# Performance work log

Hardware: AMD Instinct MI355X
Metric: run time of the kernel (lower is better)

The kernel has to match this reference:

```python
import jax, jax.numpy as jnp
import numpy as np

N = 50000      # nodes
E = 800000     # edges
IN = 128       # in_ch
OUT = 32       # out_ch
H = 4          # heads
ED = 16        # edge_dim
SLOPE = 0.2    # LeakyReLU negative slope (GATv2 default and outer activation)


def setup_inputs() -> dict:
    key = jax.random.key(0)
    ks = jax.random.split(key, 10)
    s_in = 1.0 / np.sqrt(IN)
    s_ed = 1.0 / np.sqrt(ED)
    s_out = 1.0 / np.sqrt(OUT)
    return {
        "x": jax.random.normal(ks[0], (N, IN), jnp.float32),
        "edge_index": jax.random.randint(ks[1], (2, E), 0, N, dtype=jnp.int32),
        "edges_attr": jax.random.normal(ks[2], (E, ED), jnp.float32),
        "W_l": jax.random.normal(ks[3], (IN, H * OUT), jnp.float32) * s_in,
        "b_l": jnp.zeros((H * OUT,), jnp.float32),
        "W_r": jax.random.normal(ks[4], (IN, H * OUT), jnp.float32) * s_in,
        "b_r": jnp.zeros((H * OUT,), jnp.float32),
        "W_e": jax.random.normal(ks[5], (ED, H * OUT), jnp.float32) * s_ed,
        "att": jax.random.normal(ks[6], (H, OUT), jnp.float32) * s_out,
        "bias": jnp.zeros((OUT,), jnp.float32),
    }


def reference(x, edge_index, edges_attr, W_l, b_l, W_r, b_r, W_e, att, bias):
    src, tgt = edge_index[0], edge_index[1]

    # add_self_loops with fill_value='mean': self-loop attr = scatter-mean of
    # incoming edge attrs per target node (0 for isolated nodes, as in PyG).
    deg = jax.ops.segment_sum(jnp.ones((E,), x.dtype), tgt, num_segments=N)
    attr_sum = jax.ops.segment_sum(edges_attr, tgt, num_segments=N)
    loop_attr = attr_sum / jnp.maximum(deg, 1.0)[:, None]
    node_ids = jnp.arange(N, dtype=src.dtype)
    src_f = jnp.concatenate([src, node_ids])   # [E+N]
    tgt_f = jnp.concatenate([tgt, node_ids])   # [E+N]
    attr_f = jnp.concatenate([edges_attr, loop_attr], axis=0)  # [E+N, ED]

    x_l = (x @ W_l + b_l).reshape(N, H, OUT)   # source transform
    x_r = (x @ W_r + b_r).reshape(N, H, OUT)   # target transform
    e = (attr_f @ W_e).reshape(-1, H, OUT)     # edge transform

    # GATv2 score: att . leaky_relu(x_l[j] + x_r[i] + e_ij)
    m = x_l[src_f] + x_r[tgt_f] + e                          # [E+N, H, OUT]
    scores = jnp.einsum('ehc,hc->eh', jax.nn.leaky_relu(m, SLOPE), att)

    # scatter-softmax over edges grouped by target node (every segment has a
    # self-loop, so segment_max is well-defined)
    smax = jax.ops.segment_max(scores, tgt_f, num_segments=N)
    ex = jnp.exp(scores - smax[tgt_f])
    denom = jax.ops.segment_sum(ex, tgt_f, num_segments=N)
    alpha = ex / denom[tgt_f]                                # [E+N, H]

    # weighted aggregation of source messages x_l[j]
    msg = alpha[:, :, None] * x_l[src_f]                     # [E+N, H, OUT]
    out = jax.ops.segment_sum(msg, tgt_f, num_segments=N)   # [N, H, OUT]

    out = out.mean(axis=1) + bias                            # concat=False -> head mean
    return jax.nn.leaky_relu(out, SLOPE)                     # outer LeakyReLU(0.2)
```

## Files before the change

### kernel.cpp

```cpp
#include <hip/hip_runtime.h>
#include <math.h>

#define NN 50000
#define NE 800000
#define SLOPE 0.2f
#define NB 49


__global__ void deg_kernel(const int* __restrict__ tgt, int* __restrict__ deg) {
  int e = blockIdx.x * 256 + threadIdx.x;
  if (e < NE) atomicAdd(&deg[tgt[e]], 1);
}

__global__ void partial_kernel(const int* __restrict__ deg, int* __restrict__ psum) {
  int b = blockIdx.x;
  int base = b * 1024 + threadIdx.x * 4;
  int s = 0;
  if (base + 3 < NN) {
    int4 v = *(const int4*)(deg + base);
    s = v.x + v.y + v.z + v.w;
  } else {
#pragma unroll
    for (int i = 0; i < 4; ++i)
      if (base + i < NN) s += deg[base + i];
  }
  s += __shfl_xor(s, 1);
  s += __shfl_xor(s, 2);
  s += __shfl_xor(s, 4);
  s += __shfl_xor(s, 8);
  s += __shfl_xor(s, 16);
  s += __shfl_xor(s, 32);
  __shared__ int wsum[4];
  if ((threadIdx.x & 63) == 0) wsum[threadIdx.x >> 6] = s;
  __syncthreads();
  if (threadIdx.x == 0) psum[b] = wsum[0] + wsum[1] + wsum[2] + wsum[3];
}

__global__ void scanpart_kernel(const int* __restrict__ psum, int* __restrict__ offs,
                                int* __restrict__ rowptr) {
  int lane = threadIdx.x;
  int mine = (lane < NB) ? psum[lane] : 0;
  int v = mine;
#pragma unroll
  for (int off = 1; off < 64; off <<= 1) {
    int u = __shfl_up(v, off);
    if (lane >= off) v += u;
  }
  if (lane < NB) offs[lane] = v - mine;
  if (lane == 63) rowptr[NN] = v;
}

__global__ void final_kernel(const int* __restrict__ deg, const int* __restrict__ offs,
                             int* __restrict__ rowptr, int* __restrict__ cursor) {
  int b = blockIdx.x;
  int t = threadIdx.x;
  int base = b * 1024 + t * 4;
  int d0 = 0, d1 = 0, d2 = 0, d3 = 0;
  if (base + 3 < NN) {
    int4 v = *(const int4*)(deg + base);
    d0 = v.x; d1 = v.y; d2 = v.z; d3 = v.w;
  } else {
    if (base < NN) d0 = deg[base];
    if (base + 1 < NN) d1 = deg[base + 1];
    if (base + 2 < NN) d2 = deg[base + 2];
  }
  int s = d0 + d1 + d2 + d3;
  int lane = t & 63, w = t >> 6;
  int v = s;
#pragma unroll
  for (int off = 1; off < 64; off <<= 1) {
    int u = __shfl_up(v, off);
    if (lane >= off) v += u;
  }
  __shared__ int wtot[4];
  if (lane == 63) wtot[w] = v;
  __syncthreads();
  int woff = 0;
#pragma unroll
  for (int i = 0; i < 4; ++i)
    if (i < w) woff += wtot[i];
  int run = offs[b] + woff + (v - s);
  if (base < NN)     { rowptr[base] = run;     cursor[base] = run;     run += d0; }
  if (base + 1 < NN) { rowptr[base + 1] = run; cursor[base + 1] = run; run += d1; }
  if (base + 2 < NN) { rowptr[base + 2] = run; cursor[base + 2] = run; run += d2; }
  if (base + 3 < NN) { rowptr[base + 3] = run; cursor[base + 3] = run; }
}

__global__ void scatter_kernel(const int* __restrict__ src, const int* __restrict__ tgt,
                               int* __restrict__ cursor, int2* __restrict__ csr) {
  int e = blockIdx.x * 256 + threadIdx.x;
  if (e < NE) {
    int t = tgt[e];
    int pos = atomicAdd(&cursor[t], 1);
    csr[pos] = make_int2(src[e], e);
  }
}


__launch_bounds__(256)
__global__ void gemm_kernel(const float* __restrict__ x,
                            const float* __restrict__ W_l, const float* __restrict__ b_l,
                            const float* __restrict__ W_r, const float* __restrict__ b_r,
                            float* __restrict__ x_l, float* __restrict__ x_r) {
  __shared__ float xs[64 * 68];
  __shared__ float wsm[64 * 128];
  int tid = threadIdx.x;
  int cx = tid & 31;
  int rn = tid >> 5;
  int n0 = blockIdx.x * 64;
  bool isL = (blockIdx.y == 0);
  const float* W = isL ? W_l : W_r;

  float acc[8][4];
#pragma unroll
  for (int i = 0; i < 8; ++i)
#pragma unroll
    for (int j = 0; j < 4; ++j) acc[i][j] = 0.f;

  for (int kb = 0; kb < 128; kb += 64) {
#pragma unroll
    for (int r = 0; r < 4; ++r) {
      int q = tid + r * 256;
      int n = q >> 4, k4 = q & 15;
      float4 v = make_float4(0.f, 0.f, 0.f, 0.f);
      int gn = n0 + n;
      if (gn < NN) v = *(const float4*)(x + (size_t)gn * 128 + kb + 4 * k4);
      *(float4*)&xs[n * 68 + 4 * k4] = v;
    }
#pragma unroll
    for (int r = 0; r < 8; ++r) {
      int q = tid + r * 256;
      int kk = q >> 5, c4 = q & 31;
      float4 wv = *(const float4*)(W + (size_t)(kb + kk) * 128 + 4 * c4);
      *(float4*)&wsm[kk * 128 + 4 * c4] = wv;
    }
    __syncthreads();
#pragma unroll 2
    for (int k4 = 0; k4 < 16; ++k4) {
      float4 wv[4];
#pragma unroll
      for (int kk = 0; kk < 4; ++kk)
        wv[kk] = *(const float4*)&wsm[(4 * k4 + kk) * 128 + 4 * cx];
#pragma unroll
      for (int i = 0; i < 8; ++i) {
        float4 xv = *(const float4*)&xs[(8 * rn + i) * 68 + 4 * k4];
        acc[i][0] = fmaf(xv.x, wv[0].x, acc[i][0]);
        acc[i][1] = fmaf(xv.x, wv[0].y, acc[i][1]);
        acc[i][2] = fmaf(xv.x, wv[0].z, acc[i][2]);
        acc[i][3] = fmaf(xv.x, wv[0].w, acc[i][3]);
        acc[i][0] = fmaf(xv.y, wv[1].x, acc[i][0]);
        acc[i][1] = fmaf(xv.y, wv[1].y, acc[i][1]);
        acc[i][2] = fmaf(xv.y, wv[1].z, acc[i][2]);
        acc[i][3] = fmaf(xv.y, wv[1].w, acc[i][3]);
        acc[i][0] = fmaf(xv.z, wv[2].x, acc[i][0]);
        acc[i][1] = fmaf(xv.z, wv[2].y, acc[i][1]);
        acc[i][2] = fmaf(xv.z, wv[2].z, acc[i][2]);
        acc[i][3] = fmaf(xv.z, wv[2].w, acc[i][3]);
        acc[i][0] = fmaf(xv.w, wv[3].x, acc[i][0]);
        acc[i][1] = fmaf(xv.w, wv[3].y, acc[i][1]);
        acc[i][2] = fmaf(xv.w, wv[3].z, acc[i][2]);
        acc[i][3] = fmaf(xv.w, wv[3].w, acc[i][3]);
      }
    }
    __syncthreads();
  }

  const float* bptr = isL ? b_l : b_r;
  float* optr = isL ? x_l : x_r;
  int cc = 4 * cx;
  float4 bv = *(const float4*)(bptr + cc);
#pragma unroll
  for (int i = 0; i < 8; ++i) {
    int gn = n0 + 8 * rn + i;
    if (gn < NN) {
      float4 o = make_float4(acc[i][0] + bv.x, acc[i][1] + bv.y,
                             acc[i][2] + bv.z, acc[i][3] + bv.w);
      *(float4*)(optr + (size_t)gn * 128 + cc) = o;
    }
  }
}


#define EDGE_PROC(AV, XL)                                              \
  {                                                                    \
    float e0 = AV[0] * wek[0].x;                                       \
    e0 = fmaf(AV[1], wek[1].x, e0);   e0 = fmaf(AV[2], wek[2].x, e0);  \
    e0 = fmaf(AV[3], wek[3].x, e0);   e0 = fmaf(AV[4], wek[4].x, e0);  \
    e0 = fmaf(AV[5], wek[5].x, e0);   e0 = fmaf(AV[6], wek[6].x, e0);  \
    e0 = fmaf(AV[7], wek[7].x, e0);   e0 = fmaf(AV[8], wek[8].x, e0);  \
    e0 = fmaf(AV[9], wek[9].x, e0);   e0 = fmaf(AV[10], wek[10].x, e0);\
    e0 = fmaf(AV[11], wek[11].x, e0); e0 = fmaf(AV[12], wek[12].x, e0);\
    e0 = fmaf(AV[13], wek[13].x, e0); e0 = fmaf(AV[14], wek[14].x, e0);\
    e0 = fmaf(AV[15], wek[15].x, e0);                                  \
    float e1 = AV[0] * wek[0].y;                                       \
    e1 = fmaf(AV[1], wek[1].y, e1);   e1 = fmaf(AV[2], wek[2].y, e1);  \
    e1 = fmaf(AV[3], wek[3].y, e1);   e1 = fmaf(AV[4], wek[4].y, e1);  \
    e1 = fmaf(AV[5], wek[5].y, e1);   e1 = fmaf(AV[6], wek[6].y, e1);  \
    e1 = fmaf(AV[7], wek[7].y, e1);   e1 = fmaf(AV[8], wek[8].y, e1);  \
    e1 = fmaf(AV[9], wek[9].y, e1);   e1 = fmaf(AV[10], wek[10].y, e1);\
    e1 = fmaf(AV[11], wek[11].y, e1); e1 = fmaf(AV[12], wek[12].y, e1);\
    e1 = fmaf(AV[13], wek[13].y, e1); e1 = fmaf(AV[14], wek[14].y, e1);\
    e1 = fmaf(AV[15], wek[15].y, e1);                                  \
    es0 += e0; es1 += e1;                                              \
    float m0 = (XL.x + xr.x) + e0;                                     \
    float m1 = (XL.y + xr.y) + e1;                                     \
    float lm0 = fmaf(SLOPE, fminf(m0, 0.f), fmaxf(m0, 0.f));           \
    float lm1 = fmaf(SLOPE, fminf(m1, 0.f), fmaxf(m1, 0.f));           \
    float part = fmaf(attv.y, lm1, attv.x * lm0);                      \
    part += __shfl_xor(part, 1);                                       \
    part += __shfl_xor(part, 2);                                       \
    part += __shfl_xor(part, 4);                                       \
    part += __shfl_xor(part, 8);                                       \
    float p = __expf(part);                                            \
    lh += p;                                                           \
    acc0 = fmaf(p, XL.x, acc0);                                        \
    acc1 = fmaf(p, XL.y, acc1);                                        \
  }

__launch_bounds__(256)
__global__ void gat_kernel(const float* __restrict__ x_l, const float* __restrict__ x_r,
                           const int* __restrict__ rowptr, const int2* __restrict__ csr,
                           const float* __restrict__ eattr, const float* __restrict__ W_e,
                           const float* __restrict__ att, const float* __restrict__ bias,
                           float* __restrict__ out) {
  int wid = threadIdx.x >> 6;
  int lane = threadIdx.x & 63;
  int tbase = (blockIdx.x * 4 + wid) * 4;

  float2 wek[16];
#pragma unroll
  for (int k = 0; k < 16; ++k)
    wek[k] = *(const float2*)(W_e + k * 128 + 2 * lane);
  float2 attv = *(const float2*)(att + 2 * lane);
  float bv = bias[(2 * lane) & 31];
  float bv1 = bias[((2 * lane) & 31) + 1];

  for (int tt = 0; tt < 4; ++tt) {
    int t = tbase + tt;
    float2 xr = *(const float2*)(x_r + (size_t)t * 128 + 2 * lane);
    int start = __builtin_amdgcn_readfirstlane(rowptr[t]);
    int end = __builtin_amdgcn_readfirstlane(rowptr[t + 1]);

    float lh = 0.f, acc0 = 0.f, acc1 = 0.f, es0 = 0.f, es1 = 0.f;

    int j = start;
    for (; j + 2 <= end; j += 2) {
      int2 ceA = csr[j];
      int2 ceB = csr[j + 1];
      int srcA = __builtin_amdgcn_readfirstlane(ceA.x);
      int eidA = __builtin_amdgcn_readfirstlane(ceA.y);
      int srcB = __builtin_amdgcn_readfirstlane(ceB.x);
      int eidB = __builtin_amdgcn_readfirstlane(ceB.y);
      const float* apA = eattr + (size_t)eidA * 16;
      const float* apB = eattr + (size_t)eidB * 16;
      float aA[16], aB[16];
#pragma unroll
      for (int k = 0; k < 16; ++k) aA[k] = apA[k];
#pragma unroll
      for (int k = 0; k < 16; ++k) aB[k] = apB[k];
      float2 xlA = *(const float2*)(x_l + (size_t)srcA * 128 + 2 * lane);
      float2 xlB = *(const float2*)(x_l + (size_t)srcB * 128 + 2 * lane);
      EDGE_PROC(aA, xlA)
      EDGE_PROC(aB, xlB)
    }
    if (j < end) {
      int2 ce = csr[j];
      int srcn = __builtin_amdgcn_readfirstlane(ce.x);
      int eid = __builtin_amdgcn_readfirstlane(ce.y);
      const float* ap = eattr + (size_t)eid * 16;
      float aC[16];
#pragma unroll
      for (int k = 0; k < 16; ++k) aC[k] = ap[k];
      float2 xlC = *(const float2*)(x_l + (size_t)srcn * 128 + 2 * lane);
      EDGE_PROC(aC, xlC)
    }

    {
      float rdeg = 1.0f / fmaxf((float)(end - start), 1.0f);
      float e0 = es0 * rdeg, e1 = es1 * rdeg;
      float2 xl = *(const float2*)(x_l + (size_t)t * 128 + 2 * lane);
      float m0 = (xl.x + xr.x) + e0;
      float m1 = (xl.y + xr.y) + e1;
      float lm0 = fmaf(SLOPE, fminf(m0, 0.f), fmaxf(m0, 0.f));
      float lm1 = fmaf(SLOPE, fminf(m1, 0.f), fmaxf(m1, 0.f));
      float part = fmaf(attv.y, lm1, attv.x * lm0);
      part += __shfl_xor(part, 1);
      part += __shfl_xor(part, 2);
      part += __shfl_xor(part, 4);
      part += __shfl_xor(part, 8);
      float p = __expf(part);
      lh += p;
      acc0 = fmaf(p, xl.x, acc0);
      acc1 = fmaf(p, xl.y, acc1);
    }

    float inv = 1.0f / lh;
    float v0 = acc0 * inv, v1 = acc1 * inv;
    v0 += __shfl_xor(v0, 16);
    v0 += __shfl_xor(v0, 32);
    v1 += __shfl_xor(v1, 16);
    v1 += __shfl_xor(v1, 32);
    if (lane < 16) {
      float o0 = fmaf(v0, 0.25f, bv);
      float o1 = fmaf(v1, 0.25f, bv1);
      o0 = fmaf(SLOPE, fminf(o0, 0.f), fmaxf(o0, 0.f));
      o1 = fmaf(SLOPE, fminf(o1, 0.f), fmaxf(o1, 0.f));
      *(float2*)(out + (size_t)t * 32 + 2 * lane) = make_float2(o0, o1);
    }
  }
}


extern "C" void kernel_launch(void* const* d_in, const int* in_sizes, int n_in,
                              void* d_out, int out_size, void* d_ws, size_t ws_size,
                              hipStream_t stream) {
  const float* x = (const float*)d_in[0];
  const int* ei = (const int*)d_in[1];
  const float* eattr = (const float*)d_in[2];
  const float* W_l = (const float*)d_in[3];
  const float* b_l = (const float*)d_in[4];
  const float* W_r = (const float*)d_in[5];
  const float* b_r = (const float*)d_in[6];
  const float* W_e = (const float*)d_in[7];
  const float* att = (const float*)d_in[8];
  const float* bias = (const float*)d_in[9];
  float* out = (float*)d_out;

  char* ws = (char*)d_ws;
  int2* csr = (int2*)ws;
  float* x_l = (float*)(ws + 6400000);
  float* x_r = (float*)(ws + 32000000);
  int* deg = (int*)(ws + 57600000);
  int* rowptr = (int*)(ws + 57800000);
  int* cursor = (int*)(ws + 58000016);
  int* psum = (int*)(ws + 58200016);
  int* offs = (int*)(ws + 58200512);

  hipMemsetAsync(deg, 0, NN * sizeof(int), stream);
  deg_kernel<<<(NE + 255) / 256, 256, 0, stream>>>(ei + NE, deg);
  partial_kernel<<<NB, 256, 0, stream>>>(deg, psum);
  scanpart_kernel<<<1, 64, 0, stream>>>(psum, offs, rowptr);
  final_kernel<<<NB, 256, 0, stream>>>(deg, offs, rowptr, cursor);
  scatter_kernel<<<(NE + 255) / 256, 256, 0, stream>>>(ei, ei + NE, cursor, csr);
  gemm_kernel<<<dim3((NN + 63) / 64, 2), 256, 0, stream>>>(x, W_l, b_l, W_r, b_r, x_l, x_r);
  gat_kernel<<<NN / 16, 256, 0, stream>>>(x_l, x_r, rowptr, csr, eattr, W_e, att, bias, out);
}
```

Before: 348.4 us.

## Permute edge attributes into CSR order during scatter and stream them sequentially

Result: slower. 372.9 us (+7.0%).

```diff
diff --git a/kernel.cpp b/kernel.cpp
--- a/kernel.cpp
+++ b/kernel.cpp
@@ -5,6 +5,7 @@
 #define NE 800000
 #define SLOPE 0.2f
 #define NB 49
+#define LOG2E 1.44269504f
 
 
 __global__ void deg_kernel(const int* __restrict__ tgt, int* __restrict__ deg) {
@@ -86,8 +87,28 @@
   if (base + 3 < NN) { rowptr[base + 3] = run; cursor[base + 3] = run; }
 }
 
-__global__ void scatter_kernel(const int* __restrict__ src, const int* __restrict__ tgt,
-                               int* __restrict__ cursor, int2* __restrict__ csr) {
+__global__ void scatter_attr_kernel(const int* __restrict__ src, const int* __restrict__ tgt,
+                                    const float4* __restrict__ ea4, int* __restrict__ cursor,
+                                    int* __restrict__ csr_src, float4* __restrict__ attr_csr) {
+  int e = blockIdx.x * 256 + threadIdx.x;
+  if (e < NE) {
+    float4 a0 = ea4[(size_t)e * 4 + 0];
+    float4 a1 = ea4[(size_t)e * 4 + 1];
+    float4 a2 = ea4[(size_t)e * 4 + 2];
+    float4 a3 = ea4[(size_t)e * 4 + 3];
+    int t = tgt[e];
+    int pos = atomicAdd(&cursor[t], 1);
+    csr_src[pos] = src[e];
+    size_t b = (size_t)pos * 4;
+    attr_csr[b + 0] = a0;
+    attr_csr[b + 1] = a1;
+    attr_csr[b + 2] = a2;
+    attr_csr[b + 3] = a3;
+  }
+}
+
+__global__ void scatter_eid_kernel(const int* __restrict__ src, const int* __restrict__ tgt,
+                                   int* __restrict__ cursor, int2* __restrict__ csr) {
   int e = blockIdx.x * 256 + threadIdx.x;
   if (e < NE) {
     int t = tgt[e];
@@ -176,6 +197,123 @@
       float4 o = make_float4(acc[i][0] + bv.x, acc[i][1] + bv.y,
                              acc[i][2] + bv.z, acc[i][3] + bv.w);
       *(float4*)(optr + (size_t)gn * 128 + cc) = o;
+    }
+  }
+}
+
+
+__launch_bounds__(256)
+__global__ void gat_seq_kernel(const float* __restrict__ x_l, const float* __restrict__ x_r,
+                               const int* __restrict__ rowptr, const int* __restrict__ csr_src,
+                               const float4* __restrict__ attr4, const float* __restrict__ W_e,
+                               const float* __restrict__ att, const float* __restrict__ bias,
+                               float* __restrict__ out) {
+  int wid = threadIdx.x >> 6;
+  int lane = threadIdx.x & 63;
+  int tbase = (blockIdx.x * 4 + wid) * 4;
+
+  float2 wek[16];
+#pragma unroll
+  for (int k = 0; k < 16; ++k)
+    wek[k] = *(const float2*)(W_e + k * 128 + 2 * lane);
+  float2 attv = *(const float2*)(att + 2 * lane);
+  attv.x *= LOG2E;
+  attv.y *= LOG2E;
+  float bv0 = bias[(2 * lane) & 31];
+  float bv1 = bias[((2 * lane) & 31) + 1];
+
+  for (int tt = 0; tt < 4; ++tt) {
+    int t = tbase + tt;
+    float2 xr = *(const float2*)(x_r + (size_t)t * 128 + 2 * lane);
+    int start = __builtin_amdgcn_readfirstlane(rowptr[t]);
+    int end = __builtin_amdgcn_readfirstlane(rowptr[t + 1]);
+
+    float lh = 0.f, acc0 = 0.f, acc1 = 0.f, es0 = 0.f, es1 = 0.f;
+
+    if (end > start) {
+      int s0 = __builtin_amdgcn_readfirstlane(csr_src[start]);
+      float2 xl = *(const float2*)(x_l + (size_t)s0 * 128 + 2 * lane);
+      int j1 = (start + 1 < end) ? start + 1 : start;
+      int svn = csr_src[j1];
+
+      for (int j = start; j < end; ++j) {
+        size_t ab = (size_t)j * 4;
+        float4 A0 = attr4[ab + 0];
+        float4 A1 = attr4[ab + 1];
+        float4 A2 = attr4[ab + 2];
+        float4 A3 = attr4[ab + 3];
+        int sn = __builtin_amdgcn_readfirstlane(svn);
+        float2 nxl = *(const float2*)(x_l + (size_t)sn * 128 + 2 * lane);
+        int jnn = (j + 2 < end) ? j + 2 : start;
+        svn = csr_src[jnn];
+
+        float e0 = A0.x * wek[0].x;
+        e0 = fmaf(A0.y, wek[1].x, e0);  e0 = fmaf(A0.z, wek[2].x, e0);
+        e0 = fmaf(A0.w, wek[3].x, e0);  e0 = fmaf(A1.x, wek[4].x, e0);
+        e0 = fmaf(A1.y, wek[5].x, e0);  e0 = fmaf(A1.z, wek[6].x, e0);
+        e0 = fmaf(A1.w, wek[7].x, e0);  e0 = fmaf(A2.x, wek[8].x, e0);
+        e0 = fmaf(A2.y, wek[9].x, e0);  e0 = fmaf(A2.z, wek[10].x, e0);
+        e0 = fmaf(A2.w, wek[11].x, e0); e0 = fmaf(A3.x, wek[12].x, e0);
+        e0 = fmaf(A3.y, wek[13].x, e0); e0 = fmaf(A3.z, wek[14].x, e0);
+        e0 = fmaf(A3.w, wek[15].x, e0);
+        float e1 = A0.x * wek[0].y;
+        e1 = fmaf(A0.y, wek[1].y, e1);  e1 = fmaf(A0.z, wek[2].y, e1);
+        e1 = fmaf(A0.w, wek[3].y, e1);  e1 = fmaf(A1.x, wek[4].y, e1);
+        e1 = fmaf(A1.y, wek[5].y, e1);  e1 = fmaf(A1.z, wek[6].y, e1);
+        e1 = fmaf(A1.w, wek[7].y, e1);  e1 = fmaf(A2.x, wek[8].y, e1);
+        e1 = fmaf(A2.y, wek[9].y, e1);  e1 = fmaf(A2.z, wek[10].y, e1);
+        e1 = fmaf(A2.w, wek[11].y, e1); e1 = fmaf(A3.x, wek[12].y, e1);
+        e1 = fmaf(A3.y, wek[13].y, e1); e1 = fmaf(A3.z, wek[14].y, e1);
+        e1 = fmaf(A3.w, wek[15].y, e1);
+        es0 += e0; es1 += e1;
+        float m0 = (xl.x + xr.x) + e0;
+        float m1 = (xl.y + xr.y) + e1;
+        float lm0 = fmaf(SLOPE, fminf(m0, 0.f), fmaxf(m0, 0.f));
+        float lm1 = fmaf(SLOPE, fminf(m1, 0.f), fmaxf(m1, 0.f));
+        float part = fmaf(attv.y, lm1, attv.x * lm0);
+        part += __shfl_xor(part, 1);
+        part += __shfl_xor(part, 2);
+        part += __shfl_xor(part, 4);
+        part += __shfl_xor(part, 8);
+        float p = exp2f(part);
+        lh += p;
+        acc0 = fmaf(p, xl.x, acc0);
+        acc1 = fmaf(p, xl.y, acc1);
+        xl = nxl;
+      }
+    }
+
+    {
+      float rdeg = 1.0f / fmaxf((float)(end - start), 1.0f);
+      float e0 = es0 * rdeg, e1 = es1 * rdeg;
+      float2 xl = *(const float2*)(x_l + (size_t)t * 128 + 2 * lane);
+      float m0 = (xl.x + xr.x) + e0;
+      float m1 = (xl.y + xr.y) + e1;
+      float lm0 = fmaf(SLOPE, fminf(m0, 0.f), fmaxf(m0, 0.f));
+      float lm1 = fmaf(SLOPE, fminf(m1, 0.f), fmaxf(m1, 0.f));
+      float part = fmaf(attv.y, lm1, attv.x * lm0);
+      part += __shfl_xor(part, 1);
+      part += __shfl_xor(part, 2);
+      part += __shfl_xor(part, 4);
+      part += __shfl_xor(part, 8);
+      float p = exp2f(part);
+      lh += p;
+      acc0 = fmaf(p, xl.x, acc0);
+      acc1 = fmaf(p, xl.y, acc1);
+    }
+
+    float inv = 1.0f / lh;
+    float v0 = acc0 * inv, v1 = acc1 * inv;
+    v0 += __shfl_xor(v0, 16);
+    v0 += __shfl_xor(v0, 32);
+    v1 += __shfl_xor(v1, 16);
+    v1 += __shfl_xor(v1, 32);
+    if (lane < 16) {
+      float o0 = fmaf(v0, 0.25f, bv0);
+      float o1 = fmaf(v1, 0.25f, bv1);
+      o0 = fmaf(SLOPE, fminf(o0, 0.f), fmaxf(o0, 0.f));
+      o1 = fmaf(SLOPE, fminf(o1, 0.f), fmaxf(o1, 0.f));
+      *(float2*)(out + (size_t)t * 32 + 2 * lane) = make_float2(o0, o1);
     }
   }
 }
@@ -211,18 +349,18 @@
     part += __shfl_xor(part, 2);                                       \
     part += __shfl_xor(part, 4);                                       \
     part += __shfl_xor(part, 8);                                       \
-    float p = __expf(part);                                            \
+    float p = exp2f(part);                                             \
     lh += p;                                                           \
     acc0 = fmaf(p, XL.x, acc0);                                        \
     acc1 = fmaf(p, XL.y, acc1);                                        \
   }
 
 __launch_bounds__(256)
-__global__ void gat_kernel(const float* __restrict__ x_l, const float* __restrict__ x_r,
-                           const int* __restrict__ rowptr, const int2* __restrict__ csr,
-                           const float* __restrict__ eattr, const float* __restrict__ W_e,
-                           const float* __restrict__ att, const float* __restrict__ bias,
-                           float* __restrict__ out) {
+__global__ void gat_eid_kernel(const float* __restrict__ x_l, const float* __restrict__ x_r,
+                               const int* __restrict__ rowptr, const int2* __restrict__ csr,
+                               const float* __restrict__ eattr, const float* __restrict__ W_e,
+                               const float* __restrict__ att, const float* __restrict__ bias,
+                               float* __restrict__ out) {
   int wid = threadIdx.x >> 6;
   int lane = threadIdx.x & 63;
   int tbase = (blockIdx.x * 4 + wid) * 4;
@@ -232,6 +370,8 @@
   for (int k = 0; k < 16; ++k)
     wek[k] = *(const float2*)(W_e + k * 128 + 2 * lane);
   float2 attv = *(const float2*)(att + 2 * lane);
+  attv.x *= LOG2E;
+  attv.y *= LOG2E;
   float bv = bias[(2 * lane) & 31];
   float bv1 = bias[((2 * lane) & 31) + 1];
 
@@ -288,7 +428,7 @@
       part += __shfl_xor(part, 2);
       part += __shfl_xor(part, 4);
       part += __shfl_xor(part, 8);
-      float p = __expf(part);
+      float p = exp2f(part);
       lh += p;
       acc0 = fmaf(p, xl.x, acc0);
       acc1 = fmaf(p, xl.y, acc1);
@@ -327,21 +467,46 @@
   float* out = (float*)d_out;
 
   char* ws = (char*)d_ws;
-  int2* csr = (int2*)ws;
-  float* x_l = (float*)(ws + 6400000);
-  float* x_r = (float*)(ws + 32000000);
-  int* deg = (int*)(ws + 57600000);
-  int* rowptr = (int*)(ws + 57800000);
-  int* cursor = (int*)(ws + 58000016);
-  int* psum = (int*)(ws + 58200016);
-  int* offs = (int*)(ws + 58200512);
-
-  hipMemsetAsync(deg, 0, NN * sizeof(int), stream);
-  deg_kernel<<<(NE + 255) / 256, 256, 0, stream>>>(ei + NE, deg);
-  partial_kernel<<<NB, 256, 0, stream>>>(deg, psum);
-  scanpart_kernel<<<1, 64, 0, stream>>>(psum, offs, rowptr);
-  final_kernel<<<NB, 256, 0, stream>>>(deg, offs, rowptr, cursor);
-  scatter_kernel<<<(NE + 255) / 256, 256, 0, stream>>>(ei, ei + NE, cursor, csr);
-  gemm_kernel<<<dim3((NN + 63) / 64, 2), 256, 0, stream>>>(x, W_l, b_l, W_r, b_r, x_l, x_r);
-  gat_kernel<<<NN / 16, 256, 0, stream>>>(x_l, x_r, rowptr, csr, eattr, W_e, att, bias, out);
-}
+  const size_t NEED_BIG = 106200528;
+
+  if (ws_size >= NEED_BIG) {
+    float4* attr_csr = (float4*)ws;
+    float* x_l = (float*)(ws + 51200000);
+    float* x_r = (float*)(ws + 76800000);
+    int* csr_src = (int*)(ws + 102400000);
+    int* deg = (int*)(ws + 105600000);
+    int* rowptr = (int*)(ws + 105800000);
+    int* cursor = (int*)(ws + 106000016);
+    int* psum = (int*)(ws + 106200016);
+    int* offs = (int*)(ws + 106200272);
+
+    hipMemsetAsync(deg, 0, NN * sizeof(int), stream);
+    deg_kernel<<<(NE + 255) / 256, 256, 0, stream>>>(ei + NE, deg);
+    partial_kernel<<<NB, 256, 0, stream>>>(deg, psum);
+    scanpart_kernel<<<1, 64, 0, stream>>>(psum, offs, rowptr);
+    final_kernel<<<NB, 256, 0, stream>>>(deg, offs, rowptr, cursor);
+    scatter_attr_kernel<<<(NE + 255) / 256, 256, 0, stream>>>(
+        ei, ei + NE, (const float4*)eattr, cursor, csr_src, attr_csr);
+    gemm_kernel<<<dim3(782, 2), 256, 0, stream>>>(x, W_l, b_l, W_r, b_r, x_l, x_r);
+    gat_seq_kernel<<<NN / 16, 256, 0, stream>>>(x_l, x_r, rowptr, csr_src,
+                                                (const float4*)attr_csr, W_e, att, bias, out);
+  } else {
+    int2* csr = (int2*)ws;
+    float* x_l = (float*)(ws + 6400000);
+    float* x_r = (float*)(ws + 32000000);
+    int* deg = (int*)(ws + 57600000);
+    int* rowptr = (int*)(ws + 57800000);
+    int* cursor = (int*)(ws + 58000016);
+    int* psum = (int*)(ws + 58200016);
+    int* offs = (int*)(ws + 58200512);
+
+    hipMemsetAsync(deg, 0, NN * sizeof(int), stream);
+    deg_kernel<<<(NE + 255) / 256, 256, 0, stream>>>(ei + NE, deg);
+    partial_kernel<<<NB, 256, 0, stream>>>(deg, psum);
+    scanpart_kernel<<<1, 64, 0, stream>>>(psum, offs, rowptr);
+    final_kernel<<<NB, 256, 0, stream>>>(deg, offs, rowptr, cursor);
+    scatter_eid_kernel<<<(NE + 255) / 256, 256, 0, stream>>>(ei, ei + NE, cursor, csr);
+    gemm_kernel<<<dim3(782, 2), 256, 0, stream>>>(x, W_l, b_l, W_r, b_r, x_l, x_r);
+    gat_eid_kernel<<<NN / 16, 256, 0, stream>>>(x_l, x_r, rowptr, csr, eattr, W_e, att, bias, out);
+  }
+}
```
